# Kernel optimization log

Hardware: AMD Instinct MI355X
Metric: run time of the kernel (lower is better)

Reference implementation:

```python
import jax, jax.numpy as jnp
import numpy as np


def _cdist(x, y):
    # Euclidean pairwise distances, (N,D) x (M,D) -> (N,M)
    x2 = jnp.sum(x * x, axis=1, keepdims=True)          # (N,1)
    y2 = jnp.sum(y * y, axis=1, keepdims=True).T        # (1,M)
    sq = x2 + y2 - 2.0 * (x @ y.T)
    return jnp.sqrt(jnp.maximum(sq, 0.0))


def setup_inputs() -> dict:
    key = jax.random.key(0)
    k1, k2, k3, k4 = jax.random.split(key, 4)
    return {
        "pred_feat": jax.random.normal(k1, (8192, 6), dtype=jnp.float32),
        "pred_decoder": jax.random.normal(k2, (4096, 4), dtype=jnp.float32),
        "input_data": jax.random.normal(k3, (4096, 4), dtype=jnp.float32),
        "gt_data": jax.random.normal(k4, (32768, 6), dtype=jnp.float32),
    }


def _repulsion_loss(pred_points, alpha=100.0, margin=0.3):
    N = pred_points.shape[0]
    d = _cdist(pred_points, pred_points)                # (N,N)
    eye = jnp.eye(N, dtype=d.dtype)
    d_no_self = d + 1e6 * eye
    min_dist = jnp.min(d_no_self, axis=1)               # (N,)
    penalty = jax.nn.softplus(alpha * (margin - min_dist))
    return jnp.mean(penalty ** 2)


def reference(pred_feat, pred_decoder, input_data, gt_data):
    # train_decoder=False branch of CombinedCriterionAEImpulse.forward
    pred_points = pred_feat[:, :3]
    pred_normals = pred_feat[:, 3:]
    gt_points = gt_data[:, :3]
    gt_normals = gt_data[:, 3:]

    # nearest-neighbor matching: NxL cdist + argmin + gather
    dists = _cdist(pred_points, gt_points)              # (N,L)
    min_indices = jnp.argmin(dists, axis=1)             # (N,)
    closest_gt_points = gt_points[min_indices]          # (N,3)

    attraction_loss = jnp.mean((pred_points - closest_gt_points) ** 2)
    repulsion = _repulsion_loss(pred_points)
    inlier_loss = attraction_loss + repulsion

    # normal alignment loss
    closest_gt_normals = gt_normals[min_indices]        # (N,3)
    eps = 1e-05
    pn = pred_normals / jnp.maximum(
        jnp.linalg.norm(pred_normals, axis=1, keepdims=True), eps)
    gn = closest_gt_normals / jnp.maximum(
        jnp.linalg.norm(closest_gt_normals, axis=1, keepdims=True), eps)
    cos_theta = jnp.sum(pn * gn, axis=1)
    norm_loss = jnp.mean(1.0 - cos_theta)

    combined_loss = inlier_loss + norm_loss * 10.0
    return combined_loss
```

## Files before the change

### kernel.cpp

```cpp
#include <hip/hip_runtime.h>
#include <cstdint>

typedef unsigned short ushort_t;
typedef unsigned int u32;
typedef __attribute__((ext_vector_type(8))) short bf16x8;
typedef __attribute__((ext_vector_type(16))) float f32x16;

#define N_PRED 8192
#define N_GT   32768

#define NN_WAVES  4096
#define ALL_WAVES 5120

#define O_PRA  1048576u
#define O_PRB  1310720u
#define O_CNN  1572864u
#define O_CRP  3670016u
#define O_PART 4194304u

__device__ __forceinline__ float max3f(float a, float b, float c) {
    float d;
    asm("v_max3_f32 %0, %1, %2, %3" : "=v"(d) : "v"(a), "v"(b), "v"(c));
    return d;
}
__device__ __forceinline__ ushort_t f2b(float v) {
    u32 b = __float_as_uint(v);
    return (ushort_t)((b + 0x7FFFu + ((b >> 16) & 1u)) >> 16);
}
__device__ __forceinline__ float red16(const f32x16 a, float best) {
    const float m0 = max3f(a[0], a[1], a[2]);
    const float m1 = max3f(a[3], a[4], a[5]);
    const float m2 = max3f(a[6], a[7], a[8]);
    const float m3 = max3f(a[9], a[10], a[11]);
    const float m4 = max3f(a[12], a[13], a[14]);
    const float m5 = max3f(m0, m1, a[15]);
    const float m6 = max3f(m2, m3, m4);
    return max3f(best, m5, m6);
}

__global__ __launch_bounds__(256) void k_prep(const float* __restrict__ pred,
                                              const float* __restrict__ gt,
                                              ushort_t* __restrict__ gtA,
                                              ushort_t* __restrict__ prA,
                                              ushort_t* __restrict__ prB) {
    const int i = blockIdx.x * 256 + threadIdx.x;
    if (i < N_GT) {
        const float x = gt[i * 6 + 0], y = gt[i * 6 + 1], z = gt[i * 6 + 2];
        const ushort_t xh = f2b(x), yh = f2b(y), zh = f2b(z);
        const ushort_t xl = f2b(x - __uint_as_float((u32)xh << 16));
        const ushort_t yl = f2b(y - __uint_as_float((u32)yh << 16));
        const ushort_t zl = f2b(z - __uint_as_float((u32)zh << 16));
        const float w = -0.5f * fmaf(z, z, fmaf(y, y, x * x));
        const ushort_t wh = f2b(w);
        const ushort_t wl = f2b(w - __uint_as_float((u32)wh << 16));
        ushort_t* d = gtA + (i >> 5) * 512 + (i & 31) * 8;
        d[0] = xh; d[1] = yh; d[2] = zh; d[3] = xh; d[4] = yh; d[5] = zh; d[6] = xl; d[7] = yl;
        d += 256;
        d[0] = zl; d[1] = wh; d[2] = wl; d[3] = 0; d[4] = 0; d[5] = 0; d[6] = 0; d[7] = 0;
    }
    if (i < N_PRED) {
        const float x = pred[i * 6 + 0], y = pred[i * 6 + 1], z = pred[i * 6 + 2];
        const ushort_t xh = f2b(x), yh = f2b(y), zh = f2b(z);
        const ushort_t xl = f2b(x - __uint_as_float((u32)xh << 16));
        const ushort_t yl = f2b(y - __uint_as_float((u32)yh << 16));
        const ushort_t zl = f2b(z - __uint_as_float((u32)zh << 16));
        const float w = -0.5f * fmaf(z, z, fmaf(y, y, x * x));
        const ushort_t wh = f2b(w);
        const ushort_t wl = f2b(w - __uint_as_float((u32)wh << 16));
        ushort_t* a = prA + (i >> 5) * 512 + (i & 31) * 8;
        a[0] = xh; a[1] = yh; a[2] = zh; a[3] = xh; a[4] = yh; a[5] = zh; a[6] = xl; a[7] = yl;
        a += 256;
        a[0] = zl; a[1] = wh; a[2] = wl; a[3] = 0; a[4] = 0; a[5] = 0; a[6] = 0; a[7] = 0;
        const ushort_t ONE = 0x3F80;
        ushort_t* b = prB + (i >> 5) * 512 + (i & 31) * 8;
        b[0] = xh; b[1] = yh; b[2] = zh; b[3] = xl; b[4] = yl; b[5] = zl; b[6] = xh; b[7] = yh;
        b += 256;
        b[0] = zh; b[1] = ONE; b[2] = ONE; b[3] = 0; b[4] = 0; b[5] = 0; b[6] = 0; b[7] = 0;
    }
}

__global__ __launch_bounds__(256) void k_pair(const ushort_t* __restrict__ gtA,
                                              const ushort_t* __restrict__ prA,
                                              const ushort_t* __restrict__ prB,
                                              float* __restrict__ chunkNN,
                                              float* __restrict__ chunkRP) {
    const int wid = blockIdx.x * 4 + (threadIdx.x >> 6);
    const int lane = threadIdx.x & 63;
    const f32x16 zc = {};

    const bool isNN = (wid < NN_WAVES);
    const int rw = isNN ? wid : (wid - NN_WAVES);
    const int pg = rw & 63;
    const int sp = rw >> 6;

    const int lu = (lane >> 5) * 32 + (lane & 31);

    const bf16x8* bp = (const bf16x8*)prB;
    const bf16x8 B0 = bp[(pg * 4 + 0) * 64 + lu];
    const bf16x8 B1 = bp[(pg * 4 + 1) * 64 + lu];
    const bf16x8 B2 = bp[(pg * 4 + 2) * 64 + lu];
    const bf16x8 B3 = bp[(pg * 4 + 3) * 64 + lu];

    const bf16x8* a0 = (const bf16x8*)(isNN ? gtA : prA) + sp * 1024 + lu;

    float b0 = -3.0e38f, b1 = -3.0e38f, b2 = -3.0e38f, b3 = -3.0e38f;
    bf16x8 Acur = a0[0];
#pragma unroll
    for (int t = 0; t < 16; ++t) {
        const bf16x8 Anxt = (t < 15) ? a0[(t + 1) * 64] : Acur;
        f32x16 accA = __builtin_amdgcn_mfma_f32_32x32x16_bf16(Acur, B0, zc, 0, 0, 0);
        f32x16 accB = __builtin_amdgcn_mfma_f32_32x32x16_bf16(Acur, B1, zc, 0, 0, 0);
        b0 = red16(accA, b0);
        accA = __builtin_amdgcn_mfma_f32_32x32x16_bf16(Acur, B2, zc, 0, 0, 0);
        b1 = red16(accB, b1);
        accB = __builtin_amdgcn_mfma_f32_32x32x16_bf16(Acur, B3, zc, 0, 0, 0);
        b2 = red16(accA, b2);
        b3 = red16(accB, b3);
        Acur = Anxt;
    }

    b0 = fmaxf(b0, __shfl_xor(b0, 32));
    b1 = fmaxf(b1, __shfl_xor(b1, 32));
    b2 = fmaxf(b2, __shfl_xor(b2, 32));
    b3 = fmaxf(b3, __shfl_xor(b3, 32));

    if (lane < 32) {
        const int Pb = pg * 128 + lane;
        if (isNN) {
            chunkNN[(Pb +  0) * 64 + sp] = b0;
            chunkNN[(Pb + 32) * 64 + sp] = b1;
            chunkNN[(Pb + 64) * 64 + sp] = b2;
            chunkNN[(Pb + 96) * 64 + sp] = b3;
        } else {
            chunkRP[(Pb +  0) * 16 + sp] = b0;
            chunkRP[(Pb + 32) * 16 + sp] = b1;
            chunkRP[(Pb + 64) * 16 + sp] = b2;
            chunkRP[(Pb + 96) * 16 + sp] = b3;
        }
    }
}

__global__ __launch_bounds__(256) void k_fin(const float* __restrict__ pred,
                                             const float* __restrict__ gt,
                                             const float* __restrict__ chunkNN,
                                             const float* __restrict__ chunkRP,
                                             float* __restrict__ partials) {
    const int wave = threadIdx.x >> 6;
    const int lane = threadIdx.x & 63;
    const int p = blockIdx.x * 4 + wave;

    const float px = pred[p * 6 + 0], py = pred[p * 6 + 1], pz = pred[p * 6 + 2];

    float m = chunkNN[p * 64 + lane];
    int c = lane;
#pragma unroll
    for (int off = 32; off > 0; off >>= 1) {
        const float om = __shfl_xor(m, off);
        const int   oc = __shfl_xor(c, off);
        const bool take = (om > m) || (om == m && oc < c);
        m = take ? om : m;
        c = take ? oc : c;
    }
    float bh = -3.0e38f;
    int bj = 0x7FFFFFFF;
#pragma unroll 2
    for (int i = 0; i < 8; ++i) {
        const int g = c * 512 + i * 64 + lane;
        const float x = gt[g * 6 + 0], y = gt[g * 6 + 1], z = gt[g * 6 + 2];
        const float w = -0.5f * fmaf(z, z, fmaf(y, y, x * x));
        const float h = fmaf(px, x, fmaf(py, y, fmaf(pz, z, w)));
        if (h > bh) { bh = h; bj = g; }
    }
#pragma unroll
    for (int off = 32; off > 0; off >>= 1) {
        const float oh = __shfl_xor(bh, off);
        const int   og = __shfl_xor(bj, off);
        const bool take = (oh > bh) || (oh == bh && og < bj);
        bh = take ? oh : bh;
        bj = take ? og : bj;
    }
    const int j = bj;

    const int c1 = p >> 9;
    float rm = -3.0e38f;
    int rc = 0;
    if (lane < 16 && lane != c1) { rm = chunkRP[p * 16 + lane]; rc = lane; }
#pragma unroll
    for (int off = 32; off > 0; off >>= 1) {
        const float om = __shfl_xor(rm, off);
        const int   oc = __shfl_xor(rc, off);
        const bool take = (om > rm) || (om == rm && oc < rc);
        rm = take ? om : rm;
        rc = take ? oc : rc;
    }
    float hr = -3.0e38f;
#pragma unroll 2
    for (int i = 0; i < 8; ++i) {
        const int q = c1 * 512 + i * 64 + lane;
        const float x = pred[q * 6 + 0], y = pred[q * 6 + 1], z = pred[q * 6 + 2];
        const float w = -0.5f * fmaf(z, z, fmaf(y, y, x * x));
        float h = fmaf(px, x, fmaf(py, y, fmaf(pz, z, w)));
        h = (q == p) ? -3.0e38f : h;
        hr = fmaxf(hr, h);
    }
#pragma unroll 2
    for (int i = 0; i < 8; ++i) {
        const int q = rc * 512 + i * 64 + lane;
        const float x = pred[q * 6 + 0], y = pred[q * 6 + 1], z = pred[q * 6 + 2];
        const float w = -0.5f * fmaf(z, z, fmaf(y, y, x * x));
        float h = fmaf(px, x, fmaf(py, y, fmaf(pz, z, w)));
        h = (q == p) ? -3.0e38f : h;
        hr = fmaxf(hr, h);
    }
#pragma unroll
    for (int off = 32; off > 0; off >>= 1) hr = fmaxf(hr, __shfl_xor(hr, off));

    __shared__ float red[4][3];
    if (lane == 0) {
        const float gx = gt[j * 6 + 0], gy = gt[j * 6 + 1], gz = gt[j * 6 + 2];
        const float dx = px - gx, dy = py - gy, dz = pz - gz;
        const float att = dx * dx + dy * dy + dz * dz;

        const float pnx = pred[p * 6 + 3], pny = pred[p * 6 + 4], pnz = pred[p * 6 + 5];
        const float gnx = gt[j * 6 + 3],   gny = gt[j * 6 + 4],   gnz = gt[j * 6 + 5];
        const float pl = fmaxf(sqrtf(pnx * pnx + pny * pny + pnz * pnz), 1e-5f);
        const float gl = fmaxf(sqrtf(gnx * gnx + gny * gny + gnz * gnz), 1e-5f);
        const float nrm = 1.0f - (pnx * gnx + pny * gny + pnz * gnz) / (pl * gl);

        const float pp2 = px * px + py * py + pz * pz;
        float d2 = fmaf(-2.0f, hr, pp2);
        d2 = fmaxf(d2, 0.0f);
        const float xa = 100.0f * (0.3f - sqrtf(d2));
        const float sp2 = fmaxf(xa, 0.0f) + log1pf(expf(-fabsf(xa)));

        red[wave][0] = att;
        red[wave][1] = nrm;
        red[wave][2] = sp2 * sp2;
    }
    __syncthreads();
    if (threadIdx.x < 3)
        partials[blockIdx.x * 3 + threadIdx.x] =
            red[0][threadIdx.x] + red[1][threadIdx.x] +
            red[2][threadIdx.x] + red[3][threadIdx.x];
}

__device__ __forceinline__ float wave_reduce(float v) {
#pragma unroll
    for (int off = 32; off > 0; off >>= 1) v += __shfl_down(v, off, 64);
    return v;
}

__global__ __launch_bounds__(256) void k_comb(const float* __restrict__ partials,
                                              float* __restrict__ out) {
    float a = 0.f, n = 0.f, r = 0.f;
    const int t = threadIdx.x;
#pragma unroll
    for (int k = 0; k < 8; ++k) {
        const int row = t + k * 256;
        a += partials[row * 3 + 0];
        n += partials[row * 3 + 1];
        r += partials[row * 3 + 2];
    }
    a = wave_reduce(a);
    n = wave_reduce(n);
    r = wave_reduce(r);
    __shared__ float red[3][4];
    const int wave = t >> 6, lane = t & 63;
    if (lane == 0) { red[0][wave] = a; red[1][wave] = n; red[2][wave] = r; }
    __syncthreads();
    if (t == 0) {
        const float A = red[0][0] + red[0][1] + red[0][2] + red[0][3];
        const float Nn = red[1][0] + red[1][1] + red[1][2] + red[1][3];
        const float R = red[2][0] + red[2][1] + red[2][2] + red[2][3];
        out[0] = A / (float)(N_PRED * 3) + R / (float)N_PRED + 10.0f * (Nn / (float)N_PRED);
    }
}

extern "C" void kernel_launch(void* const* d_in, const int* in_sizes, int n_in,
                              void* d_out, int out_size, void* d_ws, size_t ws_size,
                              hipStream_t stream) {
    const float* pred = (const float*)d_in[0];
    const float* gt   = (const float*)d_in[3];
    float* out = (float*)d_out;
    char* ws = (char*)d_ws;

    ushort_t* gtA = (ushort_t*)ws;
    ushort_t* prA = (ushort_t*)(ws + O_PRA);
    ushort_t* prB = (ushort_t*)(ws + O_PRB);
    float* chunkNN = (float*)(ws + O_CNN);
    float* chunkRP = (float*)(ws + O_CRP);
    float* partials = (float*)(ws + O_PART);

    k_prep<<<N_GT / 256, 256, 0, stream>>>(pred, gt, gtA, prA, prB);
    k_pair<<<ALL_WAVES / 4, 256, 0, stream>>>(gtA, prA, prB, chunkNN, chunkRP);
    k_fin<<<N_PRED / 4, 256, 0, stream>>>(pred, gt, chunkNN, chunkRP, partials);
    k_comb<<<1, 256, 0, stream>>>(partials, out);
}
```

Measured before the change: 38.86 us.

## Track winning 32-point tile in MFMA scan to shrink fp32 refinement

The pairwise MFMA scan now records which 32-column tile produced each running maximum and writes packed (score, tile) 64-bit keys. The finalize kernel then reduces keys with a single u64 max and re-evaluates only one 32-point tile in fp32, instead of a 512-point chunk. Self-distances are masked inside the diagonal MFMA tiles, so the repulsion refinement no longer needs to rescan the point's own chunk. This cuts fp32 refinement loads and ALU in k_fin. In exchange it adds compare/select work in the inner scan loop and larger key buffers, and it relies on the bf16-split score ranking the tiles correctly.

```diff
diff --git a/kernel.cpp b/kernel.cpp
--- a/kernel.cpp
+++ b/kernel.cpp
@@ -3,6 +3,7 @@
 
 typedef unsigned short ushort_t;
 typedef unsigned int u32;
+typedef unsigned long long u64;
 typedef __attribute__((ext_vector_type(8))) short bf16x8;
 typedef __attribute__((ext_vector_type(16))) float f32x16;
 
@@ -14,9 +15,9 @@
 
 #define O_PRA  1048576u
 #define O_PRB  1310720u
-#define O_CNN  1572864u
-#define O_CRP  3670016u
-#define O_PART 4194304u
+#define O_KNN  1572864u
+#define O_KRP  5767168u
+#define O_PART 6815744u
 
 __device__ __forceinline__ float max3f(float a, float b, float c) {
     float d;
@@ -27,16 +28,33 @@
     u32 b = __float_as_uint(v);
     return (ushort_t)((b + 0x7FFFu + ((b >> 16) & 1u)) >> 16);
 }
-__device__ __forceinline__ float red16(const f32x16 a, float best) {
-    const float m0 = max3f(a[0], a[1], a[2]);
-    const float m1 = max3f(a[3], a[4], a[5]);
-    const float m2 = max3f(a[6], a[7], a[8]);
-    const float m3 = max3f(a[9], a[10], a[11]);
-    const float m4 = max3f(a[12], a[13], a[14]);
-    const float m5 = max3f(m0, m1, a[15]);
-    const float m6 = max3f(m2, m3, m4);
-    return max3f(best, m5, m6);
-}
+__device__ __forceinline__ u32 packf(float v) {
+    const u32 b = __float_as_uint(v);
+    return b ^ ((u32)((int)b >> 31) | 0x80000000u);
+}
+
+#define LATCH(ACC, B, K, T)                                        \
+    {                                                              \
+        const float _m0 = max3f(ACC[0], ACC[1], ACC[2]);           \
+        const float _m1 = max3f(ACC[3], ACC[4], ACC[5]);           \
+        const float _m2 = max3f(ACC[6], ACC[7], ACC[8]);           \
+        const float _m3 = max3f(ACC[9], ACC[10], ACC[11]);         \
+        const float _m4 = max3f(ACC[12], ACC[13], ACC[14]);        \
+        const float _m5 = max3f(_m0, _m1, ACC[15]);                \
+        const float _m6 = max3f(_m2, _m3, _m4);                    \
+        const float _gm = fmaxf(_m5, _m6);                         \
+        K = (_gm > B) ? (u32)(T) : K;                              \
+        B = fmaxf(B, _gm);                                         \
+    }
+
+#define MASKROW(ACC)                                               \
+    {                                                              \
+        _Pragma("unroll")                                          \
+        for (int _r = 0; _r < 16; ++_r) {                          \
+            const int _row = (_r & 3) + 8 * (_r >> 2) + rowoff;    \
+            ACC[_r] = (_row == col) ? -3.0e38f : ACC[_r];          \
+        }                                                          \
+    }
 
 __global__ __launch_bounds__(256) void k_prep(const float* __restrict__ pred,
                                               const float* __restrict__ gt,
@@ -79,14 +97,46 @@
     }
 }
 
+template <bool DIAG>
+__device__ __forceinline__ void scan16(const bf16x8* __restrict__ ap,
+                                       const bf16x8 B0, const bf16x8 B1,
+                                       const bf16x8 B2, const bf16x8 B3,
+                                       const int ts0, const int ts1,
+                                       const int ts2, const int ts3,
+                                       const int col, const int rowoff,
+                                       float& b0, float& b1, float& b2, float& b3,
+                                       u32& k0, u32& k1, u32& k2, u32& k3) {
+    const f32x16 zc = {};
+    bf16x8 Aa = ap[0];
+    bf16x8 Ab = ap[64];
+#pragma unroll
+    for (int t = 0; t < 16; ++t) {
+        const int tn = (t + 2 < 16) ? t + 2 : 15;
+        const bf16x8 An = ap[tn * 64];
+        f32x16 accA = __builtin_amdgcn_mfma_f32_32x32x16_bf16(Aa, B0, zc, 0, 0, 0);
+        f32x16 accB = __builtin_amdgcn_mfma_f32_32x32x16_bf16(Aa, B1, zc, 0, 0, 0);
+        if (DIAG && t == ts0) MASKROW(accA);
+        LATCH(accA, b0, k0, t);
+        accA = __builtin_amdgcn_mfma_f32_32x32x16_bf16(Aa, B2, zc, 0, 0, 0);
+        if (DIAG && t == ts1) MASKROW(accB);
+        LATCH(accB, b1, k1, t);
+        accB = __builtin_amdgcn_mfma_f32_32x32x16_bf16(Aa, B3, zc, 0, 0, 0);
+        if (DIAG && t == ts2) MASKROW(accA);
+        LATCH(accA, b2, k2, t);
+        if (DIAG && t == ts3) MASKROW(accB);
+        LATCH(accB, b3, k3, t);
+        Aa = Ab;
+        Ab = An;
+    }
+}
+
 __global__ __launch_bounds__(256) void k_pair(const ushort_t* __restrict__ gtA,
                                               const ushort_t* __restrict__ prA,
                                               const ushort_t* __restrict__ prB,
-                                              float* __restrict__ chunkNN,
-                                              float* __restrict__ chunkRP) {
+                                              u64* __restrict__ keysNN,
+                                              u64* __restrict__ keysRP) {
     const int wid = blockIdx.x * 4 + (threadIdx.x >> 6);
     const int lane = threadIdx.x & 63;
-    const f32x16 zc = {};
 
     const bool isNN = (wid < NN_WAVES);
     const int rw = isNN ? wid : (wid - NN_WAVES);
@@ -94,6 +144,8 @@
     const int sp = rw >> 6;
 
     const int lu = (lane >> 5) * 32 + (lane & 31);
+    const int col = lane & 31;
+    const int rowoff = (lane >> 5) * 4;
 
     const bf16x8* bp = (const bf16x8*)prB;
     const bf16x8 B0 = bp[(pg * 4 + 0) * 64 + lu];
@@ -101,49 +153,47 @@
     const bf16x8 B2 = bp[(pg * 4 + 2) * 64 + lu];
     const bf16x8 B3 = bp[(pg * 4 + 3) * 64 + lu];
 
-    const bf16x8* a0 = (const bf16x8*)(isNN ? gtA : prA) + sp * 1024 + lu;
+    const bf16x8* ap = (const bf16x8*)(isNN ? gtA : prA) + sp * 1024 + lu;
 
     float b0 = -3.0e38f, b1 = -3.0e38f, b2 = -3.0e38f, b3 = -3.0e38f;
-    bf16x8 Acur = a0[0];
-#pragma unroll
-    for (int t = 0; t < 16; ++t) {
-        const bf16x8 Anxt = (t < 15) ? a0[(t + 1) * 64] : Acur;
-        f32x16 accA = __builtin_amdgcn_mfma_f32_32x32x16_bf16(Acur, B0, zc, 0, 0, 0);
-        f32x16 accB = __builtin_amdgcn_mfma_f32_32x32x16_bf16(Acur, B1, zc, 0, 0, 0);
-        b0 = red16(accA, b0);
-        accA = __builtin_amdgcn_mfma_f32_32x32x16_bf16(Acur, B2, zc, 0, 0, 0);
-        b1 = red16(accB, b1);
-        accB = __builtin_amdgcn_mfma_f32_32x32x16_bf16(Acur, B3, zc, 0, 0, 0);
-        b2 = red16(accA, b2);
-        b3 = red16(accB, b3);
-        Acur = Anxt;
-    }
-
-    b0 = fmaxf(b0, __shfl_xor(b0, 32));
-    b1 = fmaxf(b1, __shfl_xor(b1, 32));
-    b2 = fmaxf(b2, __shfl_xor(b2, 32));
-    b3 = fmaxf(b3, __shfl_xor(b3, 32));
+    u32 k0 = 0, k1 = 0, k2 = 0, k3 = 0;
+
+    const bool diag = (!isNN) && (sp == (pg >> 2));
+    if (diag) {
+        const int tb = (pg & 3) * 4;
+        scan16<true>(ap, B0, B1, B2, B3, tb, tb + 1, tb + 2, tb + 3,
+                     col, rowoff, b0, b1, b2, b3, k0, k1, k2, k3);
+    } else {
+        scan16<false>(ap, B0, B1, B2, B3, -1, -1, -1, -1,
+                      col, rowoff, b0, b1, b2, b3, k0, k1, k2, k3);
+    }
+
+#define FOLD(B, K)                                                  \
+    {                                                               \
+        const float _ob = __shfl_xor(B, 32);                        \
+        const u32 _ok = __shfl_xor(K, 32);                          \
+        const bool _tk = (_ob > B) || (_ob == B && _ok < K);        \
+        B = _tk ? _ob : B;                                          \
+        K = _tk ? _ok : K;                                          \
+    }
+    FOLD(b0, k0); FOLD(b1, k1); FOLD(b2, k2); FOLD(b3, k3);
+#undef FOLD
 
     if (lane < 32) {
-        const int Pb = pg * 128 + lane;
-        if (isNN) {
-            chunkNN[(Pb +  0) * 64 + sp] = b0;
-            chunkNN[(Pb + 32) * 64 + sp] = b1;
-            chunkNN[(Pb + 64) * 64 + sp] = b2;
-            chunkNN[(Pb + 96) * 64 + sp] = b3;
-        } else {
-            chunkRP[(Pb +  0) * 16 + sp] = b0;
-            chunkRP[(Pb + 32) * 16 + sp] = b1;
-            chunkRP[(Pb + 64) * 16 + sp] = b2;
-            chunkRP[(Pb + 96) * 16 + sp] = b3;
-        }
+        u64* keys = isNN ? keysNN : keysRP;
+        const int Pb = pg * 128 + col;
+        const u32 tb = (u32)(sp * 16);
+        keys[(size_t)sp * N_PRED + Pb +  0] = ((u64)packf(b0) << 32) | (u64)(~(tb + k0));
+        keys[(size_t)sp * N_PRED + Pb + 32] = ((u64)packf(b1) << 32) | (u64)(~(tb + k1));
+        keys[(size_t)sp * N_PRED + Pb + 64] = ((u64)packf(b2) << 32) | (u64)(~(tb + k2));
+        keys[(size_t)sp * N_PRED + Pb + 96] = ((u64)packf(b3) << 32) | (u64)(~(tb + k3));
     }
 }
 
 __global__ __launch_bounds__(256) void k_fin(const float* __restrict__ pred,
                                              const float* __restrict__ gt,
-                                             const float* __restrict__ chunkNN,
-                                             const float* __restrict__ chunkRP,
+                                             const u64* __restrict__ keysNN,
+                                             const u64* __restrict__ keysRP,
                                              float* __restrict__ partials) {
     const int wave = threadIdx.x >> 6;
     const int lane = threadIdx.x & 63;
@@ -151,66 +201,48 @@
 
     const float px = pred[p * 6 + 0], py = pred[p * 6 + 1], pz = pred[p * 6 + 2];
 
-    float m = chunkNN[p * 64 + lane];
-    int c = lane;
+    u64 kv = keysNN[(size_t)lane * N_PRED + p];
 #pragma unroll
     for (int off = 32; off > 0; off >>= 1) {
-        const float om = __shfl_xor(m, off);
-        const int   oc = __shfl_xor(c, off);
-        const bool take = (om > m) || (om == m && oc < c);
-        m = take ? om : m;
-        c = take ? oc : c;
-    }
-    float bh = -3.0e38f;
-    int bj = 0x7FFFFFFF;
-#pragma unroll 2
-    for (int i = 0; i < 8; ++i) {
-        const int g = c * 512 + i * 64 + lane;
+        const u64 o = __shfl_xor(kv, off);
+        kv = (o > kv) ? o : kv;
+    }
+    const u32 tile = ~((u32)kv);
+    {
+    }
+    const int g = (int)tile * 32 + (lane & 31);
+    float bh;
+    int bj;
+    {
         const float x = gt[g * 6 + 0], y = gt[g * 6 + 1], z = gt[g * 6 + 2];
         const float w = -0.5f * fmaf(z, z, fmaf(y, y, x * x));
-        const float h = fmaf(px, x, fmaf(py, y, fmaf(pz, z, w)));
-        if (h > bh) { bh = h; bj = g; }
+        bh = fmaf(px, x, fmaf(py, y, fmaf(pz, z, w)));
+        bj = g;
     }
 #pragma unroll
     for (int off = 32; off > 0; off >>= 1) {
         const float oh = __shfl_xor(bh, off);
-        const int   og = __shfl_xor(bj, off);
+        const int og = __shfl_xor(bj, off);
         const bool take = (oh > bh) || (oh == bh && og < bj);
         bh = take ? oh : bh;
         bj = take ? og : bj;
     }
     const int j = bj;
 
-    const int c1 = p >> 9;
-    float rm = -3.0e38f;
-    int rc = 0;
-    if (lane < 16 && lane != c1) { rm = chunkRP[p * 16 + lane]; rc = lane; }
+    u64 rv = (lane < 16) ? keysRP[(size_t)lane * N_PRED + p] : 0ull;
 #pragma unroll
     for (int off = 32; off > 0; off >>= 1) {
-        const float om = __shfl_xor(rm, off);
-        const int   oc = __shfl_xor(rc, off);
-        const bool take = (om > rm) || (om == rm && oc < rc);
-        rm = take ? om : rm;
-        rc = take ? oc : rc;
-    }
-    float hr = -3.0e38f;
-#pragma unroll 2
-    for (int i = 0; i < 8; ++i) {
-        const int q = c1 * 512 + i * 64 + lane;
+        const u64 o = __shfl_xor(rv, off);
+        rv = (o > rv) ? o : rv;
+    }
+    const u32 tile2 = ~((u32)rv);
+    const int q = (int)tile2 * 32 + (lane & 31);
+    float hr;
+    {
         const float x = pred[q * 6 + 0], y = pred[q * 6 + 1], z = pred[q * 6 + 2];
         const float w = -0.5f * fmaf(z, z, fmaf(y, y, x * x));
         float h = fmaf(px, x, fmaf(py, y, fmaf(pz, z, w)));
-        h = (q == p) ? -3.0e38f : h;
-        hr = fmaxf(hr, h);
-    }
-#pragma unroll 2
-    for (int i = 0; i < 8; ++i) {
-        const int q = rc * 512 + i * 64 + lane;
-        const float x = pred[q * 6 + 0], y = pred[q * 6 + 1], z = pred[q * 6 + 2];
-        const float w = -0.5f * fmaf(z, z, fmaf(y, y, x * x));
-        float h = fmaf(px, x, fmaf(py, y, fmaf(pz, z, w)));
-        h = (q == p) ? -3.0e38f : h;
-        hr = fmaxf(hr, h);
+        hr = (q == p) ? -3.0e38f : h;
     }
 #pragma unroll
     for (int off = 32; off > 0; off >>= 1) hr = fmaxf(hr, __shfl_xor(hr, off));
@@ -287,12 +319,12 @@
     ushort_t* gtA = (ushort_t*)ws;
     ushort_t* prA = (ushort_t*)(ws + O_PRA);
     ushort_t* prB = (ushort_t*)(ws + O_PRB);
-    float* chunkNN = (float*)(ws + O_CNN);
-    float* chunkRP = (float*)(ws + O_CRP);
+    u64* keysNN = (u64*)(ws + O_KNN);
+    u64* keysRP = (u64*)(ws + O_KRP);
     float* partials = (float*)(ws + O_PART);
 
     k_prep<<<N_GT / 256, 256, 0, stream>>>(pred, gt, gtA, prA, prB);
-    k_pair<<<ALL_WAVES / 4, 256, 0, stream>>>(gtA, prA, prB, chunkNN, chunkRP);
-    k_fin<<<N_PRED / 4, 256, 0, stream>>>(pred, gt, chunkNN, chunkRP, partials);
+    k_pair<<<ALL_WAVES / 4, 256, 0, stream>>>(gtA, prA, prB, keysNN, keysRP);
+    k_fin<<<N_PRED / 4, 256, 0, stream>>>(pred, gt, keysNN, keysRP, partials);
     k_comb<<<1, 256, 0, stream>>>(partials, out);
 }
```

Measured after the change: 42.33 us. +8.9%, slower.
